# Kernel optimization log

Hardware: AMD Instinct MI355X
Metric: run time of the kernel (lower is better)

Reference implementation:

```python
import jax, jax.numpy as jnp
import numpy as np

B, C, ELL, EQ, E = 1024, 128, 16, 3, 10
P3, P2, P1 = 23, 5, 1


def setup_inputs() -> dict:
    key = jax.random.key(0)
    ks = jax.random.split(key, 8)
    x = jax.random.normal(ks[0], (B, C, ELL), dtype=jnp.float32)
    # element one-hot encoding
    elem = jax.random.randint(ks[1], (B,), 0, E)
    y = jax.nn.one_hot(elem, E, dtype=jnp.float32)
    # U matrices are fixed CG-coefficient tensors (constants); random stand-ins with correct shapes
    U3 = jax.random.normal(ks[2], (EQ, ELL, ELL, ELL, P3), dtype=jnp.float32) * 0.1
    U2 = jax.random.normal(ks[3], (EQ, ELL, ELL, P2), dtype=jnp.float32) * 0.1
    U1 = jax.random.normal(ks[4], (EQ, ELL, P1), dtype=jnp.float32) * 0.1
    # learned per-element weights, init stddev 1/num_params as in the module
    w_max = jax.random.normal(ks[5], (E, P3, C), dtype=jnp.float32) / P3
    w2 = jax.random.normal(ks[6], (E, P2, C), dtype=jnp.float32) / P2
    w1 = jax.random.normal(ks[7], (E, P1, C), dtype=jnp.float32) / P1
    return {"x": x, "y": y, "U3": U3, "U2": U2, "U1": U1,
            "w_max": w_max, "w2": w2, "w1": w1}


def reference(x, y, U3, U2, U1, w_max, w2, w1):
    # per-node element weight gather (y is one-hot over elements)
    wn3 = jnp.einsum('be,ekc->bkc', y, w_max)  # (B, P3, C)
    # main contraction: 'wxvik,ekc,bci,be->bcwxv', ordered to keep intermediates small
    t = jnp.einsum('bkc,bci->bcik', wn3, x)      # (B, C, ELL, P3)
    out = jnp.einsum('wxvik,bcik->bcwxv', U3, t)  # (B, C, EQ, ELL, ELL)
    # nu = 2 step
    wn2 = jnp.einsum('be,ekc->bkc', y, w2)
    c2 = jnp.einsum('wxvk,bkc->bcwxv', U2, wn2) + out
    out = jnp.einsum('bcwxi,bci->bcwx', c2, x)    # (B, C, EQ, ELL)
    # nu = 1 step
    wn1 = jnp.einsum('be,ekc->bkc', y, w1)
    c1 = jnp.einsum('wxk,bkc->bcwx', U1, wn1) + out
    out = jnp.einsum('bcwi,bci->bcw', c1, x)      # (B, C, EQ)
    return out.reshape(out.shape[0], -1)          # (B, C*EQ)
```

## Files before the change

### kernel.cpp

```cpp
#include <hip/hip_runtime.h>

#define B_    1024
#define C_    128
#define ELL   16
#define EQ    3
#define E_    10
#define P3    23
#define P2    5
#define NSEG  176
#define RSTR  180
#define SRS   (48 * RSTR)
#define KD    28

typedef float v2f __attribute__((ext_vector_type(2)));

#define WS_CNT   0
#define WS_LIST  64
#define WS_S     65536

#define SEG_OFF_INIT {0,20,36,52,68,84,96,108,120,132,140,148,156,164,168,172}

template <int CTRL>
__device__ __forceinline__ float dpp_ror_add(float v) {
    int s = __float_as_int(v);
    int r = __builtin_amdgcn_update_dpp(s, s, CTRL, 0xF, 0xF, false);
    return v + __int_as_float(r);
}
__device__ __forceinline__ float row16_sum(float v) {
    v = dpp_ror_add<0x121>(v);
    v = dpp_ror_add<0x122>(v);
    v = dpp_ror_add<0x124>(v);
    v = dpp_ror_add<0x128>(v);
    return v;
}

__device__ void do_lists(const float* __restrict__ y, int* __restrict__ cnt_g,
                         int* __restrict__ list_g, int t) {
    __shared__ int lcnt[E_];
    if (t < E_) lcnt[t] = 0;
    __syncthreads();
    for (int r = 0; r < 4; ++r) {
        int b = t + 256 * r;
        int e = 0;
        #pragma unroll
        for (int j = 1; j < E_; ++j)
            if (y[b * E_ + j] > 0.5f) e = j;
        int slot = atomicAdd(&lcnt[e], 1);
        list_g[e * B_ + slot] = b;
    }
    __syncthreads();
    if (t < E_) {
        int c0 = lcnt[t];
        cnt_g[t] = c0;
        int last = (c0 > 0) ? list_g[t * B_ + c0 - 1] : 0;
        int cp = (c0 + 127) & ~127;
        if (cp > B_) cp = B_;
        for (int s2 = c0; s2 < cp; ++s2) list_g[t * B_ + s2] = last;
    }
}

__global__ __launch_bounds__(256, 2) void k_s(const float* __restrict__ U3,
                                              const float* __restrict__ U2,
                                              const float* __restrict__ wmax,
                                              const float* __restrict__ w2,
                                              const float* __restrict__ y,
                                              float* __restrict__ Sg,
                                              int* __restrict__ cnt_g,
                                              int* __restrict__ list_g) {
    const int t = threadIdx.x;
    if (blockIdx.x == 48) {
        if (blockIdx.y == 0 && blockIdx.z == 0) do_lists(y, cnt_g, list_g, t);
        return;
    }
    __shared__ __align__(16) float wsm[KD * 32];
    __shared__ __align__(16) float SKL[NSEG * KD];

    const int j  = blockIdx.x;
    const int e  = blockIdx.y;
    const int cq = blockIdx.z;

    for (int idx = t; idx < KD * 32; idx += 256) {
        int k = idx >> 5, cc = idx & 31, c = cq * 32 + cc;
        wsm[idx] = (k < 23) ? wmax[(e * P3 + k) * C_ + c]
                            : w2[(e * P2 + (k - 23)) * C_ + c];
    }

    if (t < NSEG) {
        const int SO[16] = SEG_OFF_INIT;
        int v = 0;
        #pragma unroll
        for (int s = 1; s < 16; ++s) v += (t >= SO[s]) ? 1 : 0;
        const int l    = t - SO[v];
        const int real = 17 - v;

        float row[KD];
        #pragma unroll
        for (int d = 0; d < KD; ++d) row[d] = 0.f;

        if (l == 0) {
            #pragma unroll
            for (int q = 0; q < P2; ++q)
                row[23 + q] = U2[(size_t)j * (ELL * P2) + v * P2 + q];
        } else if (l < real) {
            int i = v + l - 1;
            const float* pa = U3 + (size_t)j * (ELL * ELL * P3) + (v * ELL + i) * P3;
            const float* pb = U3 + (size_t)j * (ELL * ELL * P3) + (i * ELL + v) * P3;
            if (i != v) {
                #pragma unroll
                for (int k = 0; k < P3; ++k) row[k] = pa[k] + pb[k];
            } else {
                #pragma unroll
                for (int k = 0; k < P3; ++k) row[k] = pa[k];
            }
        }

        float* dst = &SKL[t * KD];
        #pragma unroll
        for (int d4 = 0; d4 < KD / 4; ++d4)
            *(float4*)(dst + 4 * d4) = make_float4(row[4 * d4], row[4 * d4 + 1],
                                                   row[4 * d4 + 2], row[4 * d4 + 3]);
    }
    __syncthreads();

    if (t >= NSEG) return;

    const int sg = t % 44;
    const int cg = t / 44;
    const int c8 = cg * 8;

    v2f acc[4][4];
    #pragma unroll
    for (int s = 0; s < 4; ++s)
        #pragma unroll
        for (int cp2 = 0; cp2 < 4; ++cp2) acc[s][cp2] = (v2f){0.f, 0.f};

    #pragma unroll
    for (int k4 = 0; k4 < KD / 4; ++k4) {
        float4 sk4[4];
        #pragma unroll
        for (int s = 0; s < 4; ++s)
            sk4[s] = *(const float4*)&SKL[(sg + 44 * s) * KD + 4 * k4];
        #pragma unroll
        for (int kk = 0; kk < 4; ++kk) {
            const int k = 4 * k4 + kk;
            float4 w0 = *(const float4*)&wsm[k * 32 + c8];
            float4 w1 = *(const float4*)&wsm[k * 32 + c8 + 4];
            v2f wp0 = {w0.x, w0.y}, wp1 = {w0.z, w0.w};
            v2f wp2 = {w1.x, w1.y}, wp3 = {w1.z, w1.w};
            #pragma unroll
            for (int s = 0; s < 4; ++s) {
                const float skv = (kk == 0) ? sk4[s].x : (kk == 1) ? sk4[s].y
                                : (kk == 2) ? sk4[s].z : sk4[s].w;
                acc[s][0] += skv * wp0;
                acc[s][1] += skv * wp1;
                acc[s][2] += skv * wp2;
                acc[s][3] += skv * wp3;
            }
        }
    }

    #pragma unroll
    for (int s = 0; s < 4; ++s) {
        const int slot = sg + 44 * s;
        #pragma unroll
        for (int cc = 0; cc < 8; ++cc) {
            const int c = cq * 32 + c8 + cc;
            Sg[(size_t)(e * C_ + c) * SRS + j * RSTR + slot] = acc[s][cc >> 1][cc & 1];
        }
    }
}

__global__ __launch_bounds__(512, 2) void k_main(
    const float* __restrict__ x, const float* __restrict__ Sg,
    const float* __restrict__ U1, const float* __restrict__ w1,
    const int* __restrict__ cnt_g, const int* __restrict__ list_g,
    float* __restrict__ out) {

    __shared__ __align__(16) float V3L[16 * RSTR];

    const int t  = threadIdx.x;
    const int bx = blockIdx.x;
    const int w  = bx % 3, c = bx / 3;
    const int e  = blockIdx.y;
    const int xx = t & 15, bs = t >> 4;
    const int cnt  = cnt_g[e];
    const int cntp = (cnt + 127) & ~127;

    {
        const float4* src = (const float4*)(Sg + (size_t)(e * C_ + c) * SRS
                                            + (size_t)w * 16 * RSTR);
        float4* dst = (float4*)V3L;
        dst[t] = src[t];
        if (t < 208) dst[512 + t] = src[512 + t];
    }
    const float v1x = U1[w * 16 + xx] * w1[e * C_ + c];
    __syncthreads();

    const float* v3p = &V3L[xx * RSTR];
    const int SO[16] = SEG_OFF_INIT;

    #pragma clang loop unroll(disable)
    for (int base = 0; base < cntp; base += 128) {
        __syncthreads();

        const int slot = base + bs * 4;
        int bidx[4];
        #pragma unroll
        for (int r = 0; r < 4; ++r) bidx[r] = list_g[e * B_ + slot + r];

        float xm[4][16];
        float xo[4];
        #pragma unroll
        for (int r = 0; r < 4; ++r) {
            const float* xb = x + ((size_t)bidx[r] * C_ + c) * ELL;
            #pragma unroll
            for (int i4 = 0; i4 < 4; ++i4) {
                float4 a = ((const float4*)xb)[i4];
                xm[r][4 * i4 + 0] = a.x; xm[r][4 * i4 + 1] = a.y;
                xm[r][4 * i4 + 2] = a.z; xm[r][4 * i4 + 3] = a.w;
            }
            xo[r] = xb[xx];
        }

        float t2[4] = {0.f, 0.f, 0.f, 0.f};
        #pragma unroll
        for (int v = 0; v < 16; ++v) {
            const int off = SO[v];
            const int nf4 = (v == 0) ? 5 : (v < 5) ? 4 : (v < 9) ? 3 : (v < 13) ? 2 : 1;
            float inner[4];
            {
                float4 u = *(const float4*)(v3p + off);
                #pragma unroll
                for (int r = 0; r < 4; ++r) {
                    float s = u.x + u.y * xm[r][v];
                    if (v + 1 <= 15) s += u.z * xm[r][v + 1];
                    if (v + 2 <= 15) s += u.w * xm[r][v + 2];
                    inner[r] = s;
                }
            }
            #pragma unroll
            for (int q = 1; q < nf4; ++q) {
                float4 u = *(const float4*)(v3p + off + 4 * q);
                const int i0 = v + 4 * q - 1;
                #pragma unroll
                for (int r = 0; r < 4; ++r) {
                    inner[r] += u.x * xm[r][i0];
                    if (i0 + 1 <= 15) inner[r] += u.y * xm[r][i0 + 1];
                    if (i0 + 2 <= 15) inner[r] += u.z * xm[r][i0 + 2];
                    if (i0 + 3 <= 15) inner[r] += u.w * xm[r][i0 + 3];
                }
            }
            #pragma unroll
            for (int r = 0; r < 4; ++r) t2[r] += xm[r][v] * inner[r];
        }

        float cv[4];
        #pragma unroll
        for (int r = 0; r < 4; ++r) cv[r] = (t2[r] + v1x) * xo[r];
        #pragma unroll
        for (int r = 0; r < 4; ++r) cv[r] = row16_sum(cv[r]);
        if (xx == 0) {
            #pragma unroll
            for (int r = 0; r < 4; ++r)
                if (slot + r < cnt)
                    out[(size_t)bidx[r] * (C_ * EQ) + c * EQ + w] = cv[r];
        }
    }
}

extern "C" void kernel_launch(void* const* d_in, const int* in_sizes, int n_in,
                              void* d_out, int out_size, void* d_ws, size_t ws_size,
                              hipStream_t stream) {
    const float* x    = (const float*)d_in[0];
    const float* y    = (const float*)d_in[1];
    const float* U3   = (const float*)d_in[2];
    const float* U2   = (const float*)d_in[3];
    const float* U1   = (const float*)d_in[4];
    const float* wmax = (const float*)d_in[5];
    const float* w2   = (const float*)d_in[6];
    const float* w1   = (const float*)d_in[7];
    float* out = (float*)d_out;
    char*  ws  = (char*)d_ws;

    int*   cnt_g  = (int*)(ws + WS_CNT);
    int*   list_g = (int*)(ws + WS_LIST);
    float* Sg     = (float*)(ws + WS_S);
    (void)ws_size;

    k_s<<<dim3(49, E_, 4), 256, 0, stream>>>(U3, U2, wmax, w2, y, Sg, cnt_g, list_g);
    k_main<<<dim3(C_ * EQ, E_), 512, 0, stream>>>(x, Sg, U1, w1, cnt_g, list_g, out);
}
```

Baseline: 127.2 us.

## Recast main quadratic-form contraction as split-bf16 MFMA GEMM per channel

The per-node quadratic form over the 176 packed x_v*x_i features is now built as a feature matrix in shared memory and multiplied against the precomputed S coefficients with 16x16x32 bf16 MFMA instructions. Three-term hi/lo bf16 splitting keeps accuracy close to fp32. One block now covers all three EQ outputs for a channel instead of one block per (channel, w). This replaces scalar FMA work with matrix-core throughput. In exchange it adds per-tile conversion and shared-memory staging work, extra syncs, and the K dimension is padded to 192.

```diff
diff --git a/kernel.cpp b/kernel.cpp
--- a/kernel.cpp
+++ b/kernel.cpp
@@ -12,13 +12,24 @@
 #define SRS   (48 * RSTR)
 #define KD    28
 
+#define MROWS 128
+#define KSL   64
+#define FSTR  72
+
 typedef float v2f __attribute__((ext_vector_type(2)));
-
-#define WS_CNT   0
-#define WS_LIST  64
-#define WS_S     65536
+using short8 = __attribute__((ext_vector_type(8))) short;
+using f32x4  = __attribute__((ext_vector_type(4))) float;
 
 #define SEG_OFF_INIT {0,20,36,52,68,84,96,108,120,132,140,148,156,164,168,172}
+
+__device__ __forceinline__ unsigned short bf16_rne(float f) {
+    unsigned int u = __float_as_uint(f);
+    unsigned int lsb = (u >> 16) & 1u;
+    return (unsigned short)((u + 0x7fffu + lsb) >> 16);
+}
+__device__ __forceinline__ float bf16_to_f(unsigned short h) {
+    return __uint_as_float(((unsigned int)h) << 16);
+}
 
 template <int CTRL>
 __device__ __forceinline__ float dpp_ror_add(float v) {
@@ -170,100 +181,136 @@
     }
 }
 
-__global__ __launch_bounds__(512, 2) void k_main(
+__global__ __launch_bounds__(256, 2) void k_main(
     const float* __restrict__ x, const float* __restrict__ Sg,
     const float* __restrict__ U1, const float* __restrict__ w1,
     const int* __restrict__ cnt_g, const int* __restrict__ list_g,
     float* __restrict__ out) {
 
-    __shared__ __align__(16) float V3L[16 * RSTR];
-
-    const int t  = threadIdx.x;
-    const int bx = blockIdx.x;
-    const int w  = bx % 3, c = bx / 3;
-    const int e  = blockIdx.y;
-    const int xx = t & 15, bs = t >> 4;
+    __shared__ __align__(16) unsigned short Fh[MROWS * FSTR];
+    __shared__ __align__(16) unsigned short Fl[MROWS * FSTR];
+    __shared__ __align__(16) unsigned short Sh[48 * FSTR];
+    __shared__ __align__(16) unsigned short Sl[48 * FSTR];
+    __shared__ __align__(16) float XL[MROWS * ELL];
+
+    const int t    = threadIdx.x;
+    const int c    = blockIdx.x;
+    const int e    = blockIdx.y;
+    const int lane = t & 63;
+    const int wv   = t >> 6;
+    const int lr   = lane & 15;
+    const int lq   = lane >> 4;
     const int cnt  = cnt_g[e];
     const int cntp = (cnt + 127) & ~127;
-
-    {
-        const float4* src = (const float4*)(Sg + (size_t)(e * C_ + c) * SRS
-                                            + (size_t)w * 16 * RSTR);
-        float4* dst = (float4*)V3L;
-        dst[t] = src[t];
-        if (t < 208) dst[512 + t] = src[512 + t];
-    }
-    const float v1x = U1[w * 16 + xx] * w1[e * C_ + c];
-    __syncthreads();
-
-    const float* v3p = &V3L[xx * RSTR];
+    const float w1ec = w1[e * C_ + c];
+    const float* sgbase = Sg + (size_t)(e * C_ + c) * SRS;
     const int SO[16] = SEG_OFF_INIT;
 
-    #pragma clang loop unroll(disable)
-    for (int base = 0; base < cntp; base += 128) {
+    const int sl = t & 63;
+    const int rg = t >> 6;
+
+    for (int base = 0; base < cntp; base += MROWS) {
+        if (base > 0) __syncthreads();
+
+        if (t < MROWS) {
+            const int b = list_g[e * B_ + base + t];
+            const float* xb = x + ((size_t)b * C_ + c) * ELL;
+            float4* dst = (float4*)&XL[t * ELL];
+            #pragma unroll
+            for (int i4 = 0; i4 < 4; ++i4) dst[i4] = ((const float4*)xb)[i4];
+        }
         __syncthreads();
 
-        const int slot = base + bs * 4;
-        int bidx[4];
-        #pragma unroll
-        for (int r = 0; r < 4; ++r) bidx[r] = list_g[e * B_ + slot + r];
-
-        float xm[4][16];
-        float xo[4];
-        #pragma unroll
-        for (int r = 0; r < 4; ++r) {
-            const float* xb = x + ((size_t)bidx[r] * C_ + c) * ELL;
-            #pragma unroll
-            for (int i4 = 0; i4 < 4; ++i4) {
-                float4 a = ((const float4*)xb)[i4];
-                xm[r][4 * i4 + 0] = a.x; xm[r][4 * i4 + 1] = a.y;
-                xm[r][4 * i4 + 2] = a.z; xm[r][4 * i4 + 3] = a.w;
-            }
-            xo[r] = xb[xx];
-        }
-
-        float t2[4] = {0.f, 0.f, 0.f, 0.f};
-        #pragma unroll
-        for (int v = 0; v < 16; ++v) {
-            const int off = SO[v];
-            const int nf4 = (v == 0) ? 5 : (v < 5) ? 4 : (v < 9) ? 3 : (v < 13) ? 2 : 1;
-            float inner[4];
+        f32x4 acc[6];
+        #pragma unroll
+        for (int ti = 0; ti < 6; ++ti) acc[ti] = (f32x4){0.f, 0.f, 0.f, 0.f};
+
+        for (int ks = 0; ks < 3; ++ks) {
+            if (ks > 0) __syncthreads();
+
             {
-                float4 u = *(const float4*)(v3p + off);
+                const int slot = ks * KSL + sl;
+                int v = 0;
                 #pragma unroll
-                for (int r = 0; r < 4; ++r) {
-                    float s = u.x + u.y * xm[r][v];
-                    if (v + 1 <= 15) s += u.z * xm[r][v + 1];
-                    if (v + 2 <= 15) s += u.w * xm[r][v + 2];
-                    inner[r] = s;
+                for (int s = 1; s < 16; ++s) v += (slot >= SO[s]) ? 1 : 0;
+                const int l    = slot - SO[v];
+                const int real = 17 - v;
+                const bool is_lin = (slot < NSEG) && (l == 0);
+                const bool is_q   = (slot < NSEG) && (l > 0) && (l < real);
+                const int  isafe  = is_q ? (v + l - 1) : 0;
+                #pragma unroll 4
+                for (int rr = 0; rr < 32; ++rr) {
+                    const int row = rg * 32 + rr;
+                    const float xv = XL[row * ELL + v];
+                    const float xi = XL[row * ELL + isafe];
+                    const float f  = is_lin ? xv : (is_q ? xv * xi : 0.f);
+                    const unsigned short h = bf16_rne(f);
+                    Fh[row * FSTR + sl] = h;
+                    Fl[row * FSTR + sl] = bf16_rne(f - bf16_to_f(h));
                 }
             }
-            #pragma unroll
-            for (int q = 1; q < nf4; ++q) {
-                float4 u = *(const float4*)(v3p + off + 4 * q);
-                const int i0 = v + 4 * q - 1;
+            {
+                #pragma unroll 4
+                for (int j2 = 0; j2 < 12; ++j2) {
+                    const int ei = t + 256 * j2;
+                    const int n  = ei >> 6;
+                    const int kl = ei & 63;
+                    const int slot2 = ks * KSL + kl;
+                    const float sv = (slot2 < NSEG) ? sgbase[n * RSTR + slot2]
+                                                    : 0.f;
+                    const unsigned short h = bf16_rne(sv);
+                    Sh[n * FSTR + kl] = h;
+                    Sl[n * FSTR + kl] = bf16_rne(sv - bf16_to_f(h));
+                }
+            }
+            __syncthreads();
+
+            #pragma unroll
+            for (int ti = 0; ti < 6; ++ti) {
+                const int tile = wv + 4 * ti;
+                const int m = tile / 3;
+                const int n = tile % 3;
+                const unsigned short* fah = &Fh[(m * 16 + lr) * FSTR];
+                const unsigned short* fal = &Fl[(m * 16 + lr) * FSTR];
+                const unsigned short* fbh = &Sh[(n * 16 + lr) * FSTR];
+                const unsigned short* fbl = &Sl[(n * 16 + lr) * FSTR];
                 #pragma unroll
-                for (int r = 0; r < 4; ++r) {
-                    inner[r] += u.x * xm[r][i0];
-                    if (i0 + 1 <= 15) inner[r] += u.y * xm[r][i0 + 1];
-                    if (i0 + 2 <= 15) inner[r] += u.z * xm[r][i0 + 2];
-                    if (i0 + 3 <= 15) inner[r] += u.w * xm[r][i0 + 3];
+                for (int kst = 0; kst < 2; ++kst) {
+                    const int ko = kst * 32 + lq * 8;
+                    short8 ah = *(const short8*)(fah + ko);
+                    short8 al = *(const short8*)(fal + ko);
+                    short8 bh = *(const short8*)(fbh + ko);
+                    short8 bl = *(const short8*)(fbl + ko);
+                    acc[ti] = __builtin_amdgcn_mfma_f32_16x16x32_bf16(
+                                  ah, bh, acc[ti], 0, 0, 0);
+                    acc[ti] = __builtin_amdgcn_mfma_f32_16x16x32_bf16(
+                                  ah, bl, acc[ti], 0, 0, 0);
+                    acc[ti] = __builtin_amdgcn_mfma_f32_16x16x32_bf16(
+                                  al, bh, acc[ti], 0, 0, 0);
                 }
             }
-            #pragma unroll
-            for (int r = 0; r < 4; ++r) t2[r] += xm[r][v] * inner[r];
-        }
-
-        float cv[4];
-        #pragma unroll
-        for (int r = 0; r < 4; ++r) cv[r] = (t2[r] + v1x) * xo[r];
-        #pragma unroll
-        for (int r = 0; r < 4; ++r) cv[r] = row16_sum(cv[r]);
-        if (xx == 0) {
-            #pragma unroll
-            for (int r = 0; r < 4; ++r)
-                if (slot + r < cnt)
-                    out[(size_t)bidx[r] * (C_ * EQ) + c * EQ + w] = cv[r];
+        }
+
+        #pragma unroll
+        for (int ti = 0; ti < 6; ++ti) {
+            const int tile = wv + 4 * ti;
+            const int m = tile / 3;
+            const int n = tile % 3;
+            const float v1x = U1[n * 16 + lr] * w1ec;
+            #pragma unroll
+            for (int reg = 0; reg < 4; ++reg) {
+                const int row = m * 16 + lq * 4 + reg;
+                const float xmv = XL[row * ELL + lr];
+                float cv = (acc[ti][reg] + v1x) * xmv;
+                cv = row16_sum(cv);
+                if (lr == 0) {
+                    const int gslot = base + row;
+                    if (gslot < cnt) {
+                        const int b = list_g[e * B_ + gslot];
+                        out[(size_t)b * (C_ * EQ) + c * EQ + n] = cv;
+                    }
+                }
+            }
         }
     }
 }
@@ -282,11 +329,11 @@
     float* out = (float*)d_out;
     char*  ws  = (char*)d_ws;
 
-    int*   cnt_g  = (int*)(ws + WS_CNT);
-    int*   list_g = (int*)(ws + WS_LIST);
-    float* Sg     = (float*)(ws + WS_S);
+    int*   cnt_g  = (int*)(ws + 0);
+    int*   list_g = (int*)(ws + 64);
+    float* Sg     = (float*)(ws + 65536);
     (void)ws_size;
 
     k_s<<<dim3(49, E_, 4), 256, 0, stream>>>(U3, U2, wmax, w2, y, Sg, cnt_g, list_g);
-    k_main<<<dim3(C_ * EQ, E_), 512, 0, stream>>>(x, Sg, U1, w1, cnt_g, list_g, out);
-}
+    k_main<<<dim3(C_, E_), 256, 0, stream>>>(x, Sg, U1, w1, cnt_g, list_g, out);
+}
```

New measurement: 173.3 us. 36.2% more time.
